# Kernel tuning notes

Hardware: AMD Instinct MI355X
Metric: run time of the kernel (lower is better)

Reference implementation:

```python
import jax, jax.numpy as jnp
import numpy as np

EMBED_DIM = 2048
NUM_HEAD = 32
NUM_GROUP = 8
B, S = 2, 2048


def setup_inputs() -> dict:
    key = jax.random.key(0)
    ks = jax.random.split(key, 9)
    D = EMBED_DIM // NUM_HEAD
    kv_dim = NUM_GROUP * D
    s = 0.02
    return {
        "x": jax.random.normal(ks[0], (B, S, EMBED_DIM), dtype=jnp.float32),
        "wq_w": jax.random.normal(ks[1], (EMBED_DIM, EMBED_DIM), dtype=jnp.float32) * s,
        "wq_b": jnp.zeros((EMBED_DIM,), dtype=jnp.float32),
        "wk_w": jax.random.normal(ks[2], (kv_dim, EMBED_DIM), dtype=jnp.float32) * s,
        "wk_b": jnp.zeros((kv_dim,), dtype=jnp.float32),
        "wv_w": jax.random.normal(ks[3], (kv_dim, EMBED_DIM), dtype=jnp.float32) * s,
        "wv_b": jnp.zeros((kv_dim,), dtype=jnp.float32),
        "out_w": jax.random.normal(ks[4], (EMBED_DIM, EMBED_DIM), dtype=jnp.float32) * s,
        "out_b": jnp.zeros((EMBED_DIM,), dtype=jnp.float32),
    }


def reference(x, wq_w, wq_b, wk_w, wk_b, wv_w, wv_b, out_w, out_b):
    b, s, e = x.shape
    H, G = NUM_HEAD, NUM_GROUP
    D = e // H
    r = H // G  # repeat_times
    # projections (torch Linear: x @ W.T + b)
    q = (x @ wq_w.T + wq_b).reshape(b, s, H, D)
    k = (x @ wk_w.T + wk_b).reshape(b, s, G, D)
    v = (x @ wv_w.T + wv_b).reshape(b, s, G, D)
    # faithful to torch.concat([data]*r, dim=2): TILE along head axis
    # (q-head h uses kv-head h mod G)
    k = jnp.concatenate([k] * r, axis=2)  # [b, s, H, D]
    v = jnp.concatenate([v] * r, axis=2)
    # [b, H, s_q, s_k]
    scores = jnp.einsum("bqhd,bkhd->bhqk", q, k) / (D ** 0.5)
    # faithful to F.softmax(dim=1): softmax over the HEAD axis
    attn = jax.nn.softmax(scores, axis=1)
    o = jnp.einsum("bhqk,bkhd->bqhd", attn, v).reshape(b, s, e)
    return o @ out_w.T + out_b
```

## Files before the change

### kernel.cpp

```cpp
#include <hip/hip_runtime.h>


typedef unsigned short u16;
typedef unsigned int u32;
typedef __attribute__((ext_vector_type(8))) __bf16 bf16x8;
typedef __attribute__((ext_vector_type(4))) float f32x4;
typedef __attribute__((ext_vector_type(4))) float float4_t;

#define GLD16(ldsp, gp)                                                  \
  __builtin_amdgcn_global_load_lds(                                      \
      (__attribute__((address_space(1))) void*)(void*)(gp),              \
      (__attribute__((address_space(3))) void*)(void*)(ldsp), 16, 0, 0)

static __device__ __forceinline__ u16 f2bf(float f) {
  union { float f; u32 u; } v; v.f = f;
  u32 u = v.u;
  u32 r = (u + 0x7fffu + ((u >> 16) & 1u)) >> 16;
  return (u16)r;
}

static __device__ __forceinline__ bf16x8 ld8(const u16* p) {
  return *(const bf16x8*)p;
}

static __device__ __forceinline__ float hsum4(float v) {
  v += __builtin_bit_cast(float, __builtin_amdgcn_update_dpp(
           0, __builtin_bit_cast(int, v), 0x124, 0xf, 0xf, true));
  v += __builtin_bit_cast(float, __builtin_amdgcn_update_dpp(
           0, __builtin_bit_cast(int, v), 0x128, 0xf, 0xf, true));
  return v;
}

__global__ void cvt_bf16(const float* __restrict__ in, u16* __restrict__ out, int n8) {
  int i = blockIdx.x * blockDim.x + threadIdx.x;
  int stride = gridDim.x * blockDim.x;
  for (; i < n8; i += stride) {
    const float4_t* p = (const float4_t*)in + (size_t)i * 2;
    float4_t a = p[0], b = p[1];
    u32 w0 = (u32)f2bf(a[0]) | ((u32)f2bf(a[1]) << 16);
    u32 w1 = (u32)f2bf(a[2]) | ((u32)f2bf(a[3]) << 16);
    u32 w2 = (u32)f2bf(b[0]) | ((u32)f2bf(b[1]) << 16);
    u32 w3 = (u32)f2bf(b[2]) | ((u32)f2bf(b[3]) << 16);
    *(uint4*)(out + (size_t)i * 8) = make_uint4(w0, w1, w2, w3);
  }
}

template <int MODE>
__global__ __launch_bounds__(256, 2)
void gemm_bt(const u16* __restrict__ A, const u16* __restrict__ Bw,
             const float* __restrict__ bias,
             u16* __restrict__ Cb, float* __restrict__ Cf, int N) {
  constexpr int K = 2048;
  constexpr int SHSZ = (MODE == 2) ? (128 * 136) : 8192;
  __shared__ u16 sh[SHSZ];
  u16* As = sh;
  u16* Bs = sh + 4096;
  const int tid = threadIdx.x;
  const int lane = tid & 63;
  const int w = tid >> 6;
  const int m0 = blockIdx.y * 128;
  const int n0 = blockIdx.x * 128;
  const int wr = (w >> 1) * 64, wc = (w & 1) * 64;
  const int r15 = lane & 15, kq = lane >> 4;

  f32x4 acc[4][4] = {};

  for (int k0 = 0; k0 < K; k0 += 32) {
#pragma unroll
    for (int i = 0; i < 2; ++i) {
      int c = i * 256 + tid;
      int r = c >> 2, ch = c & 3;
      int sc = (ch ^ (r & 3)) * 8;
      GLD16(&As[c * 8], &A[(size_t)(m0 + r) * K + k0 + sc]);
      GLD16(&Bs[c * 8], &Bw[(size_t)(n0 + r) * K + k0 + sc]);
    }
    __syncthreads();
    bf16x8 af[4], bfr[4];
#pragma unroll
    for (int mt = 0; mt < 4; ++mt) {
      int r = wr + mt * 16 + r15;
      af[mt] = ld8(&As[r * 32 + ((kq ^ (r15 & 3)) * 8)]);
    }
#pragma unroll
    for (int nt = 0; nt < 4; ++nt) {
      int r = wc + nt * 16 + r15;
      bfr[nt] = ld8(&Bs[r * 32 + ((kq ^ (r15 & 3)) * 8)]);
    }
#pragma unroll
    for (int mt = 0; mt < 4; ++mt)
#pragma unroll
      for (int nt = 0; nt < 4; ++nt)
        acc[mt][nt] = __builtin_amdgcn_mfma_f32_16x16x32_bf16(af[mt], bfr[nt], acc[mt][nt], 0, 0, 0);
    __syncthreads();
  }

  if constexpr (MODE == 2) {
#pragma unroll
    for (int mt = 0; mt < 4; ++mt)
#pragma unroll
      for (int nt = 0; nt < 4; ++nt) {
        int col = wc + nt * 16 + r15;
        float bv = bias[n0 + col];
#pragma unroll
        for (int r = 0; r < 4; ++r) {
          int row = wr + mt * 16 + kq * 4 + r;
          sh[col * 136 + row] = f2bf(acc[mt][nt][r] + bv);
        }
      }
    __syncthreads();
    const int m0l = m0 & 2047;
    const int bb = m0 >> 11;
#pragma unroll
    for (int i = 0; i < 8; ++i) {
      int c = i * 256 + tid;
      int cc = c >> 4, so = c & 15;
      int X = cc * 136 + (so >> 2) * 32 + (so & 3) * 4;
      u32 A0 = *(const u32*)&sh[X + 0];
      u32 A1 = *(const u32*)&sh[X + 2];
      u32 B0 = *(const u32*)&sh[X + 16];
      u32 B1 = *(const u32*)&sh[X + 18];
      u32 w0 = __builtin_amdgcn_perm(B0, A0, 0x05040100u);
      u32 w1 = __builtin_amdgcn_perm(B0, A0, 0x07060302u);
      u32 w2 = __builtin_amdgcn_perm(B1, A1, 0x05040100u);
      u32 w3 = __builtin_amdgcn_perm(B1, A1, 0x07060302u);
      *(uint4*)&Cb[(size_t)(bb * 512 + n0 + cc) * 2048 + m0l + so * 8] =
          make_uint4(w0, w1, w2, w3);
    }
  } else {
    const int rb = kq * 4;
#pragma unroll
    for (int mt = 0; mt < 4; ++mt) {
#pragma unroll
      for (int nt = 0; nt < 4; ++nt) {
        int col = n0 + wc + nt * 16 + r15;
        float bv = bias[col];
#pragma unroll
        for (int r = 0; r < 4; ++r) {
          int row = m0 + wr + mt * 16 + rb + r;
          float v = acc[mt][nt][r] + bv;
          if constexpr (MODE == 0) Cb[(size_t)row * N + col] = f2bf(v);
          else                     Cf[(size_t)row * N + col] = v;
        }
      }
    }
  }
}

__global__ __launch_bounds__(1024, 4)
void attn_fused(const u16* __restrict__ Q, const u16* __restrict__ Kg,
                const u16* __restrict__ Vt, u16* __restrict__ O) {
  __shared__ float slab[8 * 528];
  __shared__ float rsb[16 * 36];

  const int tid = threadIdx.x;
  const int lane = tid & 63, w = tid >> 6;
  const int g = w & 7, zd = w >> 3;
  const int l15 = lane & 15, kq = lane >> 4;
  const int qr = l15 & 3, hl = l15 >> 2;

  const int xcd = blockIdx.x & 7;
  const int b = xcd >> 2;
  const int q0 = ((((blockIdx.x >> 3) << 2) + (xcd & 3)) << 4);
  const int qbase = q0 + zd * 8;

  const u16* Qb = Q + (size_t)b * 2048 * 2048;
  const u16* Kb = Kg + (size_t)b * 2048 * 512;
  const u16* Vb = Vt + (size_t)b * 512 * 2048;

  bf16x8 qf[2][2];
#pragma unroll
  for (int qq = 0; qq < 2; ++qq)
#pragma unroll
    for (int t = 0; t < 2; ++t)
      qf[qq][t] = ld8(&Qb[(size_t)(qbase + qq * 4 + qr) * 2048 +
                          (g + 8 * hl) * 64 + t * 32 + kq * 8]);

  f32x4 acc[2][4] = {};

  for (int k0 = 0; k0 < 2048; k0 += 32) {
    bf16x8 kf[2][2];
#pragma unroll
    for (int ko = 0; ko < 2; ++ko)
#pragma unroll
      for (int t = 0; t < 2; ++t)
        kf[ko][t] = ld8(&Kb[(size_t)(k0 + ko * 16 + l15) * 512 +
                            g * 64 + t * 32 + kq * 8]);

    f32x4 sc[2][2];
#pragma unroll
    for (int qq = 0; qq < 2; ++qq)
#pragma unroll
      for (int ko = 0; ko < 2; ++ko) {
        f32x4 s = {};
        s = __builtin_amdgcn_mfma_f32_16x16x32_bf16(kf[ko][0], qf[qq][0], s, 0, 0, 0);
        s = __builtin_amdgcn_mfma_f32_16x16x32_bf16(kf[ko][1], qf[qq][1], s, 0, 0, 0);
#pragma unroll
        for (int r = 0; r < 4; ++r) s[r] = exp2f(s[r] * 0.18033688f);
        sc[qq][ko] = s;
      }

#pragma unroll
    for (int qq = 0; qq < 2; ++qq)
#pragma unroll
      for (int ko = 0; ko < 2; ++ko) {
#pragma unroll
        for (int r = 0; r < 4; ++r) {
          float su = hsum4(sc[qq][ko][r]);
          if (hl == 0)
            slab[g * 528 + (zd * 8 + qq * 4 + qr) * 33 + ko * 16 + kq * 4 + r] = su;
        }
      }

    bf16x8 vb[4];
#pragma unroll
    for (int nt = 0; nt < 4; ++nt)
      vb[nt] = ld8(&Vb[(size_t)(g * 64 + nt * 16 + l15) * 2048 + k0 + kq * 8]);

    __syncthreads();

    if (tid < 512) {
      int q = tid >> 5, k = tid & 31;
      float s = 0.f;
#pragma unroll
      for (int gg = 0; gg < 8; ++gg) s += slab[gg * 528 + q * 33 + k];
      rsb[q * 36 + k] = __builtin_amdgcn_rcpf(s);
    }
    __syncthreads();

#pragma unroll
    for (int qq = 0; qq < 2; ++qq) {
      const int ql = zd * 8 + qq * 4 + qr;
      f32x4 rs0 = *(const f32x4*)&rsb[ql * 36 + 0 * 16 + kq * 4];
      f32x4 rs1 = *(const f32x4*)&rsb[ql * 36 + 1 * 16 + kq * 4];
      u32 paw[4];
#pragma unroll
      for (int r = 0; r < 4; ++r)
        paw[r] = (u32)f2bf(sc[qq][0][r] * rs0[r]) |
                 ((u32)f2bf(sc[qq][1][r] * rs1[r]) << 16);
      bf16x8 pa = __builtin_bit_cast(bf16x8, *(uint4*)paw);
#pragma unroll
      for (int nt = 0; nt < 4; ++nt)
        acc[qq][nt] = __builtin_amdgcn_mfma_f32_16x16x32_bf16(pa, vb[nt], acc[qq][nt], 0, 0, 0);
    }
  }

#pragma unroll
  for (int qq = 0; qq < 2; ++qq)
#pragma unroll
    for (int nt = 0; nt < 4; ++nt)
#pragma unroll
      for (int r = 0; r < 4; ++r)
        O[(size_t)(b * 2048 + qbase + qq * 4 + r) * 2048 +
          (g + 8 * kq) * 64 + nt * 16 + l15] = f2bf(acc[qq][nt][r]);
}

extern "C" void kernel_launch(void* const* d_in, const int* in_sizes, int n_in,
                              void* d_out, int out_size, void* d_ws, size_t ws_size,
                              hipStream_t stream) {
  (void)in_sizes; (void)n_in; (void)out_size; (void)ws_size;
  const float* x    = (const float*)d_in[0];
  const float* wq_w = (const float*)d_in[1];
  const float* wq_b = (const float*)d_in[2];
  const float* wk_w = (const float*)d_in[3];
  const float* wk_b = (const float*)d_in[4];
  const float* wv_w = (const float*)d_in[5];
  const float* wv_b = (const float*)d_in[6];
  const float* wo_w = (const float*)d_in[7];
  const float* wo_b = (const float*)d_in[8];
  float* out = (float*)d_out;

  char* p = (char*)d_ws;
  u16* xb  = (u16*)p; p += (size_t)4096 * 2048 * 2;
  u16* wqb = (u16*)p; p += (size_t)2048 * 2048 * 2;
  u16* wkb = (u16*)p; p += (size_t)512 * 2048 * 2;
  u16* wvb = (u16*)p; p += (size_t)512 * 2048 * 2;
  u16* wob = (u16*)p; p += (size_t)2048 * 2048 * 2;
  u16* Qb  = (u16*)p; p += (size_t)4096 * 2048 * 2;
  u16* Kb  = (u16*)p; p += (size_t)4096 * 512 * 2;
  u16* Vtb = (u16*)p; p += (size_t)1024 * 2048 * 2;
  u16* Ob  = (u16*)p; p += (size_t)4096 * 2048 * 2;

  auto cvt = [&](const float* in, u16* o, int n) {
    int n8 = n / 8;
    int grid = (n8 + 255) / 256; if (grid > 2048) grid = 2048;
    hipLaunchKernelGGL(cvt_bf16, dim3(grid), dim3(256), 0, stream, in, o, n8);
  };
  cvt(x, xb, 4096 * 2048);
  cvt(wq_w, wqb, 2048 * 2048);
  cvt(wk_w, wkb, 512 * 2048);
  cvt(wv_w, wvb, 512 * 2048);
  cvt(wo_w, wob, 2048 * 2048);

  hipLaunchKernelGGL((gemm_bt<0>), dim3(16, 32), dim3(256), 0, stream,
                     xb, wqb, wq_b, Qb, (float*)nullptr, 2048);
  hipLaunchKernelGGL((gemm_bt<0>), dim3(4, 32),  dim3(256), 0, stream,
                     xb, wkb, wk_b, Kb, (float*)nullptr, 512);
  hipLaunchKernelGGL((gemm_bt<2>), dim3(4, 32),  dim3(256), 0, stream,
                     xb, wvb, wv_b, Vtb, (float*)nullptr, 512);

  hipLaunchKernelGGL(attn_fused, dim3(256), dim3(1024), 0, stream, Qb, Kb, Vtb, Ob);

  hipLaunchKernelGGL((gemm_bt<1>), dim3(16, 32), dim3(256), 0, stream,
                     Ob, wob, wo_b, (u16*)nullptr, out, 2048);
}
```

Baseline: 448.0 us.

## Prefetch K tiles, fold softmax scale into K projection, merge conversion launches

The attention loop is restructured into a two-stage step that double-buffers the K fragments, prefetching the next tile while the current one is processed, and issues the V loads earlier. The softmax scale times log2(e) is folded into the K projection epilogue, so the attention kernel uses a raw hardware exp2 with no multiply. Packed bf16 conversion now goes through v_cvt_pk_bf16_f32, and __syncthreads is replaced by a bare barrier that waits only on LDS counters. The five fp32-to-bf16 conversion launches are merged into one kernel. Rounding K after scaling and using the hardware exp2 change numerics slightly.

```diff
diff --git a/kernel.cpp b/kernel.cpp
--- a/kernel.cpp
+++ b/kernel.cpp
@@ -21,6 +21,30 @@
 
 static __device__ __forceinline__ bf16x8 ld8(const u16* p) {
   return *(const bf16x8*)p;
+}
+
+#if __has_builtin(__builtin_amdgcn_exp2f)
+static __device__ __forceinline__ float fexp2(float x) {
+  return __builtin_amdgcn_exp2f(x);
+}
+#else
+static __device__ __forceinline__ float fexp2(float x) {
+  float r;
+  asm("v_exp_f32 %0, %1\n\ts_nop 0" : "=v"(r) : "v"(x));
+  return r;
+}
+#endif
+
+static __device__ __forceinline__ u32 cvtpk(float a, float b) {
+  u32 r;
+  asm("v_cvt_pk_bf16_f32 %0, %1, %2" : "=v"(r) : "v"(a), "v"(b));
+  return r;
+}
+
+static __device__ __forceinline__ void barrier_lgkm() {
+  asm volatile("s_waitcnt lgkmcnt(0)" ::: "memory");
+  __builtin_amdgcn_s_barrier();
+  asm volatile("" ::: "memory");
 }
 
 static __device__ __forceinline__ float hsum4(float v) {
@@ -31,17 +55,29 @@
   return v;
 }
 
-__global__ void cvt_bf16(const float* __restrict__ in, u16* __restrict__ out, int n8) {
+__global__ void cvt_all(const float* __restrict__ x, const float* __restrict__ wq,
+                        const float* __restrict__ wk, const float* __restrict__ wv,
+                        const float* __restrict__ wo, u16* __restrict__ xb,
+                        u16* __restrict__ wqb, u16* __restrict__ wkb,
+                        u16* __restrict__ wvb, u16* __restrict__ wob) {
   int i = blockIdx.x * blockDim.x + threadIdx.x;
-  int stride = gridDim.x * blockDim.x;
-  for (; i < n8; i += stride) {
-    const float4_t* p = (const float4_t*)in + (size_t)i * 2;
+  const int stride = gridDim.x * blockDim.x;
+  for (; i < 2359296; i += stride) {
+    const float* src;
+    u16* dst;
+    int j;
+    if (i < 1048576)      { src = x;  dst = xb;  j = i; }
+    else if (i < 1572864) { src = wq; dst = wqb; j = i - 1048576; }
+    else if (i < 1703936) { src = wk; dst = wkb; j = i - 1572864; }
+    else if (i < 1835008) { src = wv; dst = wvb; j = i - 1703936; }
+    else                  { src = wo; dst = wob; j = i - 1835008; }
+    const float4_t* p = (const float4_t*)src + (size_t)j * 2;
     float4_t a = p[0], b = p[1];
     u32 w0 = (u32)f2bf(a[0]) | ((u32)f2bf(a[1]) << 16);
     u32 w1 = (u32)f2bf(a[2]) | ((u32)f2bf(a[3]) << 16);
     u32 w2 = (u32)f2bf(b[0]) | ((u32)f2bf(b[1]) << 16);
     u32 w3 = (u32)f2bf(b[2]) | ((u32)f2bf(b[3]) << 16);
-    *(uint4*)(out + (size_t)i * 8) = make_uint4(w0, w1, w2, w3);
+    *(uint4*)(dst + (size_t)j * 8) = make_uint4(w0, w1, w2, w3);
   }
 }
 
@@ -49,7 +85,7 @@
 __global__ __launch_bounds__(256, 2)
 void gemm_bt(const u16* __restrict__ A, const u16* __restrict__ Bw,
              const float* __restrict__ bias,
-             u16* __restrict__ Cb, float* __restrict__ Cf, int N) {
+             u16* __restrict__ Cb, float* __restrict__ Cf, int N, float scale) {
   constexpr int K = 2048;
   constexpr int SHSZ = (MODE == 2) ? (128 * 136) : 8192;
   __shared__ u16 sh[SHSZ];
@@ -137,7 +173,7 @@
 #pragma unroll
         for (int r = 0; r < 4; ++r) {
           int row = m0 + wr + mt * 16 + rb + r;
-          float v = acc[mt][nt][r] + bv;
+          float v = (acc[mt][nt][r] + bv) * scale;
           if constexpr (MODE == 0) Cb[(size_t)row * N + col] = f2bf(v);
           else                     Cf[(size_t)row * N + col] = v;
         }
@@ -176,47 +212,57 @@
                           (g + 8 * hl) * 64 + t * 32 + kq * 8]);
 
   f32x4 acc[2][4] = {};
-
-  for (int k0 = 0; k0 < 2048; k0 += 32) {
-    bf16x8 kf[2][2];
-#pragma unroll
-    for (int ko = 0; ko < 2; ++ko)
-#pragma unroll
-      for (int t = 0; t < 2; ++t)
-        kf[ko][t] = ld8(&Kb[(size_t)(k0 + ko * 16 + l15) * 512 +
-                            g * 64 + t * 32 + kq * 8]);
-
+  bf16x8 kfA[2][2], kfB[2][2];
+
+#pragma unroll
+  for (int ko = 0; ko < 2; ++ko)
+#pragma unroll
+    for (int t = 0; t < 2; ++t)
+      kfA[ko][t] = ld8(&Kb[(size_t)(ko * 16 + l15) * 512 + g * 64 + t * 32 + kq * 8]);
+
+  auto tilestep = [&](int k0, bf16x8 (&kfC)[2][2], bf16x8 (&kfN)[2][2]) {
     f32x4 sc[2][2];
 #pragma unroll
     for (int qq = 0; qq < 2; ++qq)
 #pragma unroll
       for (int ko = 0; ko < 2; ++ko) {
         f32x4 s = {};
-        s = __builtin_amdgcn_mfma_f32_16x16x32_bf16(kf[ko][0], qf[qq][0], s, 0, 0, 0);
-        s = __builtin_amdgcn_mfma_f32_16x16x32_bf16(kf[ko][1], qf[qq][1], s, 0, 0, 0);
-#pragma unroll
-        for (int r = 0; r < 4; ++r) s[r] = exp2f(s[r] * 0.18033688f);
+        s = __builtin_amdgcn_mfma_f32_16x16x32_bf16(kfC[ko][0], qf[qq][0], s, 0, 0, 0);
+        s = __builtin_amdgcn_mfma_f32_16x16x32_bf16(kfC[ko][1], qf[qq][1], s, 0, 0, 0);
         sc[qq][ko] = s;
       }
 
+    const int kn = (k0 + 32) & 2047;
+#pragma unroll
+    for (int ko = 0; ko < 2; ++ko)
+#pragma unroll
+      for (int t = 0; t < 2; ++t)
+        kfN[ko][t] = ld8(&Kb[(size_t)(kn + ko * 16 + l15) * 512 + g * 64 + t * 32 + kq * 8]);
+
+    bf16x8 vb[4];
+#pragma unroll
+    for (int nt = 0; nt < 4; ++nt)
+      vb[nt] = ld8(&Vb[(size_t)(g * 64 + nt * 16 + l15) * 2048 + k0 + kq * 8]);
+
 #pragma unroll
     for (int qq = 0; qq < 2; ++qq)
 #pragma unroll
-      for (int ko = 0; ko < 2; ++ko) {
+      for (int ko = 0; ko < 2; ++ko)
+#pragma unroll
+        for (int r = 0; r < 4; ++r)
+          sc[qq][ko][r] = fexp2(sc[qq][ko][r]);
+#pragma unroll
+    for (int qq = 0; qq < 2; ++qq)
+#pragma unroll
+      for (int ko = 0; ko < 2; ++ko)
 #pragma unroll
         for (int r = 0; r < 4; ++r) {
           float su = hsum4(sc[qq][ko][r]);
           if (hl == 0)
             slab[g * 528 + (zd * 8 + qq * 4 + qr) * 33 + ko * 16 + kq * 4 + r] = su;
         }
-      }
-
-    bf16x8 vb[4];
-#pragma unroll
-    for (int nt = 0; nt < 4; ++nt)
-      vb[nt] = ld8(&Vb[(size_t)(g * 64 + nt * 16 + l15) * 2048 + k0 + kq * 8]);
-
-    __syncthreads();
+
+    barrier_lgkm();
 
     if (tid < 512) {
       int q = tid >> 5, k = tid & 31;
@@ -225,23 +271,28 @@
       for (int gg = 0; gg < 8; ++gg) s += slab[gg * 528 + q * 33 + k];
       rsb[q * 36 + k] = __builtin_amdgcn_rcpf(s);
     }
-    __syncthreads();
+
+    barrier_lgkm();
 
 #pragma unroll
     for (int qq = 0; qq < 2; ++qq) {
       const int ql = zd * 8 + qq * 4 + qr;
-      f32x4 rs0 = *(const f32x4*)&rsb[ql * 36 + 0 * 16 + kq * 4];
-      f32x4 rs1 = *(const f32x4*)&rsb[ql * 36 + 1 * 16 + kq * 4];
+      f32x4 rs0 = *(const f32x4*)&rsb[ql * 36 + kq * 4];
+      f32x4 rs1 = *(const f32x4*)&rsb[ql * 36 + 16 + kq * 4];
       u32 paw[4];
 #pragma unroll
       for (int r = 0; r < 4; ++r)
-        paw[r] = (u32)f2bf(sc[qq][0][r] * rs0[r]) |
-                 ((u32)f2bf(sc[qq][1][r] * rs1[r]) << 16);
+        paw[r] = cvtpk(sc[qq][0][r] * rs0[r], sc[qq][1][r] * rs1[r]);
       bf16x8 pa = __builtin_bit_cast(bf16x8, *(uint4*)paw);
 #pragma unroll
       for (int nt = 0; nt < 4; ++nt)
         acc[qq][nt] = __builtin_amdgcn_mfma_f32_16x16x32_bf16(pa, vb[nt], acc[qq][nt], 0, 0, 0);
     }
+  };
+
+  for (int k0 = 0; k0 < 2048; k0 += 64) {
+    tilestep(k0, kfA, kfB);
+    tilestep(k0 + 32, kfB, kfA);
   }
 
 #pragma unroll
@@ -280,26 +331,19 @@
   u16* Vtb = (u16*)p; p += (size_t)1024 * 2048 * 2;
   u16* Ob  = (u16*)p; p += (size_t)4096 * 2048 * 2;
 
-  auto cvt = [&](const float* in, u16* o, int n) {
-    int n8 = n / 8;
-    int grid = (n8 + 255) / 256; if (grid > 2048) grid = 2048;
-    hipLaunchKernelGGL(cvt_bf16, dim3(grid), dim3(256), 0, stream, in, o, n8);
-  };
-  cvt(x, xb, 4096 * 2048);
-  cvt(wq_w, wqb, 2048 * 2048);
-  cvt(wk_w, wkb, 512 * 2048);
-  cvt(wv_w, wvb, 512 * 2048);
-  cvt(wo_w, wob, 2048 * 2048);
-
+  hipLaunchKernelGGL(cvt_all, dim3(2048), dim3(256), 0, stream,
+                     x, wq_w, wk_w, wv_w, wo_w, xb, wqb, wkb, wvb, wob);
+
+  const float kscale = 0.125f * 1.44269504f;
   hipLaunchKernelGGL((gemm_bt<0>), dim3(16, 32), dim3(256), 0, stream,
-                     xb, wqb, wq_b, Qb, (float*)nullptr, 2048);
+                     xb, wqb, wq_b, Qb, (float*)nullptr, 2048, 1.0f);
   hipLaunchKernelGGL((gemm_bt<0>), dim3(4, 32),  dim3(256), 0, stream,
-                     xb, wkb, wk_b, Kb, (float*)nullptr, 512);
+                     xb, wkb, wk_b, Kb, (float*)nullptr, 512, kscale);
   hipLaunchKernelGGL((gemm_bt<2>), dim3(4, 32),  dim3(256), 0, stream,
-                     xb, wvb, wv_b, Vtb, (float*)nullptr, 512);
+                     xb, wvb, wv_b, Vtb, (float*)nullptr, 512, 1.0f);
 
   hipLaunchKernelGGL(attn_fused, dim3(256), dim3(1024), 0, stream, Qb, Kb, Vtb, Ob);
 
   hipLaunchKernelGGL((gemm_bt<1>), dim3(16, 32), dim3(256), 0, stream,
-                     Ob, wob, wo_b, (u16*)nullptr, out, 2048);
-}
+                     Ob, wob, wo_b, (u16*)nullptr, out, 2048, 1.0f);
+}
```

New measurement: 474.2 us. 1.06x slower.
